# Kernel optimization log

Measured on AMD Instinct MI355X. Metric: run time of the kernel, lower is better.

The kernel has to match this reference:

```python
import jax, jax.numpy as jnp
import numpy as np

D_MODEL = 1024
N_HEADS = 16
HEAD_DIM = D_MODEL // N_HEADS


def setup_inputs() -> dict:
    key = jax.random.key(0)
    ks = jax.random.split(key, 9)
    s = 0.02
    return {
        "x": jax.random.normal(ks[0], (2, 2048, D_MODEL), jnp.float32),
        "Wk": jax.random.normal(ks[1], (D_MODEL, D_MODEL), jnp.float32) * s,
        "bk": jnp.zeros((D_MODEL,), jnp.float32),
        "Wq": jax.random.normal(ks[2], (D_MODEL, D_MODEL), jnp.float32) * s,
        "bq": jnp.zeros((D_MODEL,), jnp.float32),
        "Wv": jax.random.normal(ks[3], (D_MODEL, D_MODEL), jnp.float32) * s,
        "bv": jnp.zeros((D_MODEL,), jnp.float32),
        "Wp": jax.random.normal(ks[4], (D_MODEL, D_MODEL), jnp.float32) * s,
        "bp": jnp.zeros((D_MODEL,), jnp.float32),
    }


def reference(x, Wk, bk, Wq, bq, Wv, bv, Wp, bp):
    B, T, C = x.shape
    H, Dh = N_HEADS, HEAD_DIM
    # linear projections; torch Linear: y = x @ W.T + b
    def split_heads(y):
        return y.reshape(B, T, H, Dh).transpose(0, 2, 1, 3)  # [B,H,T,Dh]
    k = split_heads(x @ Wk.T + bk)
    q = split_heads(x @ Wq.T + bq)
    v = split_heads(x @ Wv.T + bv)
    scale = 1.0 / jnp.sqrt(jnp.asarray(Dh, x.dtype))
    att = jnp.einsum("bhqd,bhkd->bhqk", q, k) * scale  # [B,H,T,T]
    causal = jnp.tril(jnp.ones((T, T), bool))
    att = jnp.where(causal[None, None], att, -jnp.inf)
    att = jax.nn.softmax(att, axis=-1)
    y = jnp.einsum("bhqk,bhkd->bhqd", att, v)  # [B,H,T,Dh]
    y = y.transpose(0, 2, 1, 3).reshape(B, T, C)
    return y @ Wp.T + bp
```

## Files before the change

### kernel.cpp

```cpp
#include <hip/hip_runtime.h>
#include <stdint.h>

typedef unsigned short u16;
typedef __bf16 bf16x8_t __attribute__((ext_vector_type(8)));
typedef float f32x4 __attribute__((ext_vector_type(4)));

#define T_LEN 2048
#define NHEADS 16
#define DHEAD 64
#define DMODEL 1024
#define QSCALE 0.1803368801111f

__device__ __forceinline__ u16 f2bf(float f) {
  union { float f; uint32_t u; } v; v.f = f;
  uint32_t r = v.u + 0x7FFFu + ((v.u >> 16) & 1u);
  return (u16)(r >> 16);
}

__device__ __forceinline__ void gload16(const u16* g, u16* l) {
  __builtin_amdgcn_global_load_lds((const __attribute__((address_space(1))) void*)g,
                                   (__attribute__((address_space(3))) void*)l, 16, 0, 0);
}

__global__ void cvt_bf16_k(const float* __restrict__ s, u16* __restrict__ d, int n) {
  int i = (blockIdx.x * blockDim.x + threadIdx.x) * 4;
  if (i >= n) return;
  float4 f = *(const float4*)(s + i);
  u16 o[4] = { f2bf(f.x), f2bf(f.y), f2bf(f.z), f2bf(f.w) };
  *(uint2*)(d + i) = *(const uint2*)o;
}

__global__ void cvt_w_k(const float* __restrict__ wq, const float* __restrict__ wk,
                        const float* __restrict__ wv, const float* __restrict__ wp,
                        u16* __restrict__ dqkv, u16* __restrict__ dp) {
  int which = blockIdx.y;
  const float* s = which == 0 ? wq : (which == 1 ? wk : (which == 2 ? wv : wp));
  u16* d = which == 3 ? dp : dqkv + (size_t)which * 1048576;
  int i = (blockIdx.x * blockDim.x + threadIdx.x) * 4;
  float4 f = *(const float4*)(s + i);
  u16 o[4] = { f2bf(f.x), f2bf(f.y), f2bf(f.z), f2bf(f.w) };
  *(uint2*)(d + i) = *(const uint2*)o;
}

template <int TM, int TN, int MODE>
__global__ __launch_bounds__(256, 3) void gemm_k(
    const u16* __restrict__ A, const u16* __restrict__ Bw,
    const float* __restrict__ b0, const float* __restrict__ b1, const float* __restrict__ b2,
    void* __restrict__ o0, void* __restrict__ o1, void* __restrict__ o2,
    int M, int N, int K)
{
  __shared__ __align__(16) u16 As[TM][64];
  __shared__ __align__(16) u16 Bs[TN][64];
  const int m0 = blockIdx.x * TM, n0 = blockIdx.y * TN;
  const int tid = threadIdx.x, lane = tid & 63, w = tid >> 6;
  const int col = lane & 15, quad = lane >> 4;
  constexpr int WM = TM / 2, WN = TN / 2;
  const int wm = (w >> 1) * WM, wn = (w & 1) * WN;
  constexpr int NI = WM / 16, NJ = WN / 16;
  const int rsub = lane >> 3;
  const int csw = ((lane & 7) ^ rsub) * 8;
  const int rx8 = col & 7;

  f32x4 acc[NI][NJ] = {};

  for (int k0 = 0; k0 < K; k0 += 64) {
    __syncthreads();
#pragma unroll
    for (int i = 0; i < TM / 32; i++) {
      int rb = (i * 4 + w) * 8;
      gload16(&A[(size_t)(m0 + rb + rsub) * K + k0 + csw], &As[rb][0]);
    }
#pragma unroll
    for (int i = 0; i < TN / 32; i++) {
      int rb = (i * 4 + w) * 8;
      gload16(&Bw[(size_t)(n0 + rb + rsub) * K + k0 + csw], &Bs[rb][0]);
    }
    __syncthreads();
#pragma unroll
    for (int s = 0; s < 2; s++) {
      bf16x8_t af[NI], bfr[NJ];
#pragma unroll
      for (int i = 0; i < NI; i++) {
        int cp = (quad ^ rx8) ^ (s * 4);
        af[i] = *(const bf16x8_t*)&As[wm + i * 16 + col][cp * 8];
      }
#pragma unroll
      for (int j = 0; j < NJ; j++) {
        int cp = (quad ^ rx8) ^ (s * 4);
        bfr[j] = *(const bf16x8_t*)&Bs[wn + j * 16 + col][cp * 8];
      }
#pragma unroll
      for (int i = 0; i < NI; i++)
#pragma unroll
        for (int j = 0; j < NJ; j++)
          acc[i][j] = __builtin_amdgcn_mfma_f32_16x16x32_bf16(af[i], bfr[j], acc[i][j], 0, 0, 0);
    }
  }

#pragma unroll
  for (int i = 0; i < NI; i++) {
#pragma unroll
    for (int j = 0; j < NJ; j++) {
      int ncol = n0 + wn + j * 16 + col;
      if (MODE == 0) {
        float bias = b0[ncol];
#pragma unroll
        for (int r = 0; r < 4; r++) {
          int m = m0 + wm + i * 16 + quad * 4 + r;
          ((float*)o0)[(size_t)m * N + ncol] = acc[i][j][r] + bias;
        }
      } else {
        int sect = ncol >> 10, nc = ncol & 1023;
        const float* bp = sect == 0 ? b0 : (sect == 1 ? b1 : b2);
        u16* op = sect == 0 ? (u16*)o0 : (sect == 1 ? (u16*)o1 : (u16*)o2);
        float bias = bp[nc];
        float scal = sect == 0 ? QSCALE : 1.0f;
        int h = nc >> 6, d = nc & 63;
#pragma unroll
        for (int r = 0; r < 4; r++) {
          int m = m0 + wm + i * 16 + quad * 4 + r;
          int b = m >> 11, t = m & 2047;
          float v = (acc[i][j][r] + bias) * scal;
          size_t idx = sect < 2 ? ((((size_t)(b * NHEADS + h)) * T_LEN + t) * DHEAD + d)
                                : ((((size_t)(b * NHEADS + h)) * DHEAD + d) * T_LEN + t);
          op[idx] = f2bf(v);
        }
      }
    }
  }
}

__global__ __launch_bounds__(256, 3) void attn_k(
    const u16* __restrict__ Q, const u16* __restrict__ Kb,
    const u16* __restrict__ Vt, u16* __restrict__ Y)
{
  __shared__ __align__(16) u16 Ks[2][64][64];
  __shared__ __align__(16) u16 Vs[2][64][64];
  __shared__ __align__(16) u16 Ps[4][16][68];
  const int bid = blockIdx.x;
  const int bh = (bid & 7) * 4 + ((bid >> 3) & 3);
  const int qt = 31 - (bid >> 5);
  const int tid = threadIdx.x, lane = tid & 63, w = tid >> 6;
  const int col = lane & 15, quad = lane >> 4;
  const int b = bh >> 4, h = bh & 15;
  const int qw = qt * 64 + w * 16;

  const int rsub = lane >> 3;
  const int csw = ((lane & 7) ^ rsub) * 8;
  const u16* kgb = Kb + (size_t)bh * T_LEN * DHEAD;
  const u16* vgb = Vt + (size_t)bh * DHEAD * T_LEN;
  const int rx = col & 7;

  bf16x8_t qf0, qf1;
  {
    const u16* p = Q + ((size_t)bh * T_LEN + qw + col) * DHEAD + quad * 8;
    qf0 = *(const bf16x8_t*)p;
    qf1 = *(const bf16x8_t*)(p + 32);
  }

  float lsum[4] = {0.f, 0.f, 0.f, 0.f};
  f32x4 o[4] = {};
  int qrow[4];
#pragma unroll
  for (int r = 0; r < 4; r++) qrow[r] = qw + quad * 4 + r;

#pragma unroll
  for (int half = 0; half < 2; half++) {
    int rb = w * 16 + half * 8;
    gload16(kgb + (size_t)(rb + rsub) * DHEAD + csw, &Ks[0][rb][0]);
    gload16(vgb + (size_t)(rb + rsub) * T_LEN + csw, &Vs[0][rb][0]);
  }

  for (int kt = 0; kt <= qt; ++kt) {
    const int k0 = kt * 64;
    const int bufi = kt & 1;
    __syncthreads();
    if (kt < qt) {
      const int k0n = k0 + 64, bn = bufi ^ 1;
#pragma unroll
      for (int half = 0; half < 2; half++) {
        int rb = w * 16 + half * 8;
        gload16(kgb + (size_t)(k0n + rb + rsub) * DHEAD + csw, &Ks[bn][rb][0]);
        gload16(vgb + (size_t)(rb + rsub) * T_LEN + k0n + csw, &Vs[bn][rb][0]);
      }
    }

    f32x4 s[4];
#pragma unroll
    for (int nt = 0; nt < 4; nt++) {
      const u16* krow = &Ks[bufi][nt * 16 + col][0];
      bf16x8_t kf0 = *(const bf16x8_t*)(krow + ((quad ^ rx) & 7) * 8);
      bf16x8_t kf1 = *(const bf16x8_t*)(krow + (((4 + quad) ^ rx) & 7) * 8);
      f32x4 a = {};
      a = __builtin_amdgcn_mfma_f32_16x16x32_bf16(qf0, kf0, a, 0, 0, 0);
      a = __builtin_amdgcn_mfma_f32_16x16x32_bf16(qf1, kf1, a, 0, 0, 0);
      s[nt] = a;
    }

    const bool diag = (kt == qt);
#pragma unroll
    for (int r = 0; r < 4; r++) {
#pragma unroll
      for (int nt = 0; nt < 4; nt++) {
        float p = __builtin_amdgcn_exp2f(s[nt][r]);
        if (diag && (k0 + nt * 16 + col) > qrow[r]) p = 0.f;
        uint32_t pu = __float_as_uint(p) & 0xFFFF0000u;
        lsum[r] += __uint_as_float(pu);
        Ps[w][quad * 4 + r][nt * 16 + col] = (u16)(pu >> 16);
      }
    }

#pragma unroll
    for (int ks = 0; ks < 2; ks++) {
      bf16x8_t pf = *(const bf16x8_t*)&Ps[w][col][ks * 32 + quad * 8];
#pragma unroll
      for (int dt = 0; dt < 4; dt++) {
        const u16* vrow = &Vs[bufi][dt * 16 + col][0];
        bf16x8_t vv = *(const bf16x8_t*)(vrow + (((ks * 4 + quad) ^ rx) & 7) * 8);
        o[dt] = __builtin_amdgcn_mfma_f32_16x16x32_bf16(pf, vv, o[dt], 0, 0, 0);
      }
    }
  }

#pragma unroll
  for (int r = 0; r < 4; r++) {
#pragma unroll
    for (int off = 1; off < 16; off <<= 1)
      lsum[r] += __shfl_xor(lsum[r], off);
    float inv = 1.0f / lsum[r];
    int t = qw + quad * 4 + r;
#pragma unroll
    for (int dt = 0; dt < 4; dt++)
      Y[((size_t)(b * T_LEN + t)) * DMODEL + h * DHEAD + dt * 16 + col] =
          f2bf(o[dt][r] * inv);
  }
}

extern "C" void kernel_launch(void* const* d_in, const int* in_sizes, int n_in,
                              void* d_out, int out_size, void* d_ws, size_t ws_size,
                              hipStream_t stream) {
  const float* x  = (const float*)d_in[0];
  const float* Wk = (const float*)d_in[1];
  const float* bk = (const float*)d_in[2];
  const float* Wq = (const float*)d_in[3];
  const float* bq = (const float*)d_in[4];
  const float* Wv = (const float*)d_in[5];
  const float* bv = (const float*)d_in[6];
  const float* Wp = (const float*)d_in[7];
  const float* bp = (const float*)d_in[8];

  char* ws = (char*)d_ws;
  const size_t MB = 1u << 20;
  u16* xb    = (u16*)(ws);
  u16* wqkv  = (u16*)(ws + 8 * MB);
  u16* wpb   = (u16*)(ws + 14 * MB);
  u16* qb    = (u16*)(ws + 16 * MB);
  u16* kb    = (u16*)(ws + 24 * MB);
  u16* vtb   = (u16*)(ws + 32 * MB);
  u16* yatt  = (u16*)(ws + 40 * MB);

  cvt_bf16_k<<<4096, 256, 0, stream>>>(x, xb, 4194304);
  dim3 gw(1024, 4);
  cvt_w_k<<<gw, 256, 0, stream>>>(Wq, Wk, Wv, Wp, wqkv, wpb);

  dim3 gqkv(32, 24);
  gemm_k<128, 128, 3><<<gqkv, 256, 0, stream>>>(xb, wqkv, bq, bk, bv,
                                                qb, kb, vtb, 4096, 3072, 1024);

  attn_k<<<1024, 256, 0, stream>>>(qb, kb, vtb, yatt);

  dim3 gp(32, 16);
  gemm_k<128, 64, 0><<<gp, 256, 0, stream>>>(yatt, wpb, bp, nullptr, nullptr,
                                             d_out, nullptr, nullptr, 4096, 1024, 1024);
}
```

Before: 182.2 us.

## Keep attention probabilities in registers via transposed MFMA, drop LDS P staging

QK^T is now computed transposed (K as the A operand), so each lane holds the scores for one query across 16 keys. These scores are packed directly into the B operand of the PV MFMA. This removes the per-wave Ps shared-memory round trip, its write/read traffic and LDS footprint. V is now read as two 8-byte pieces per fragment to match the permuted key order, and the output is written as 4-element vector stores. Launch bounds are raised to 4 blocks per CU because shared memory is smaller, which risks register pressure or spills.

```diff
diff --git a/kernel.cpp b/kernel.cpp
--- a/kernel.cpp
+++ b/kernel.cpp
@@ -130,13 +130,12 @@
   }
 }
 
-__global__ __launch_bounds__(256, 3) void attn_k(
+__global__ __launch_bounds__(256, 4) void attn_k(
     const u16* __restrict__ Q, const u16* __restrict__ Kb,
     const u16* __restrict__ Vt, u16* __restrict__ Y)
 {
   __shared__ __align__(16) u16 Ks[2][64][64];
   __shared__ __align__(16) u16 Vs[2][64][64];
-  __shared__ __align__(16) u16 Ps[4][16][68];
   const int bid = blockIdx.x;
   const int bh = (bid & 7) * 4 + ((bid >> 3) & 3);
   const int qt = 31 - (bid >> 5);
@@ -158,11 +157,9 @@
     qf1 = *(const bf16x8_t*)(p + 32);
   }
 
-  float lsum[4] = {0.f, 0.f, 0.f, 0.f};
+  const int qr = qw + col;
+  float ls[4] = {0.f, 0.f, 0.f, 0.f};
   f32x4 o[4] = {};
-  int qrow[4];
-#pragma unroll
-  for (int r = 0; r < 4; r++) qrow[r] = qw + quad * 4 + r;
 
 #pragma unroll
   for (int half = 0; half < 2; half++) {
@@ -192,47 +189,56 @@
       bf16x8_t kf0 = *(const bf16x8_t*)(krow + ((quad ^ rx) & 7) * 8);
       bf16x8_t kf1 = *(const bf16x8_t*)(krow + (((4 + quad) ^ rx) & 7) * 8);
       f32x4 a = {};
-      a = __builtin_amdgcn_mfma_f32_16x16x32_bf16(qf0, kf0, a, 0, 0, 0);
-      a = __builtin_amdgcn_mfma_f32_16x16x32_bf16(qf1, kf1, a, 0, 0, 0);
+      a = __builtin_amdgcn_mfma_f32_16x16x32_bf16(kf0, qf0, a, 0, 0, 0);
+      a = __builtin_amdgcn_mfma_f32_16x16x32_bf16(kf1, qf1, a, 0, 0, 0);
       s[nt] = a;
     }
 
     const bool diag = (kt == qt);
+    u16 pb[4][4];
+#pragma unroll
+    for (int nt = 0; nt < 4; nt++) {
+#pragma unroll
+      for (int r = 0; r < 4; r++) {
+        float p = __builtin_amdgcn_exp2f(s[nt][r]);
+        if (diag && (k0 + nt * 16 + quad * 4 + r) > qr) p = 0.f;
+        uint32_t pu = __float_as_uint(p) & 0xFFFF0000u;
+        ls[r] += __uint_as_float(pu);
+        pb[nt][r] = (u16)(pu >> 16);
+      }
+    }
+    union PU { bf16x8_t v; u16 h[8]; } pf[2];
 #pragma unroll
     for (int r = 0; r < 4; r++) {
-#pragma unroll
-      for (int nt = 0; nt < 4; nt++) {
-        float p = __builtin_amdgcn_exp2f(s[nt][r]);
-        if (diag && (k0 + nt * 16 + col) > qrow[r]) p = 0.f;
-        uint32_t pu = __float_as_uint(p) & 0xFFFF0000u;
-        lsum[r] += __uint_as_float(pu);
-        Ps[w][quad * 4 + r][nt * 16 + col] = (u16)(pu >> 16);
-      }
+      pf[0].h[r] = pb[0][r]; pf[0].h[4 + r] = pb[1][r];
+      pf[1].h[r] = pb[2][r]; pf[1].h[4 + r] = pb[3][r];
     }
 
 #pragma unroll
     for (int ks = 0; ks < 2; ks++) {
-      bf16x8_t pf = *(const bf16x8_t*)&Ps[w][col][ks * 32 + quad * 8];
 #pragma unroll
       for (int dt = 0; dt < 4; dt++) {
         const u16* vrow = &Vs[bufi][dt * 16 + col][0];
-        bf16x8_t vv = *(const bf16x8_t*)(vrow + (((ks * 4 + quad) ^ rx) & 7) * 8);
-        o[dt] = __builtin_amdgcn_mfma_f32_16x16x32_bf16(pf, vv, o[dt], 0, 0, 0);
-      }
-    }
-  }
-
-#pragma unroll
-  for (int r = 0; r < 4; r++) {
-#pragma unroll
-    for (int off = 1; off < 16; off <<= 1)
-      lsum[r] += __shfl_xor(lsum[r], off);
-    float inv = 1.0f / lsum[r];
-    int t = qw + quad * 4 + r;
-#pragma unroll
-    for (int dt = 0; dt < 4; dt++)
-      Y[((size_t)(b * T_LEN + t)) * DMODEL + h * DHEAD + dt * 16 + col] =
-          f2bf(o[dt][r] * inv);
+        union VU { bf16x8_t v; uint2 u2[2]; } va;
+        va.u2[0] = *(const uint2*)(vrow + ((ks * 4 + (quad >> 1)) ^ rx) * 8 + (quad & 1) * 4);
+        va.u2[1] = *(const uint2*)(vrow + ((ks * 4 + 2 + (quad >> 1)) ^ rx) * 8 + (quad & 1) * 4);
+        o[dt] = __builtin_amdgcn_mfma_f32_16x16x32_bf16(va.v, pf[ks].v, o[dt], 0, 0, 0);
+      }
+    }
+  }
+
+  float lsum = (ls[0] + ls[1]) + (ls[2] + ls[3]);
+  lsum += __shfl_xor(lsum, 16);
+  lsum += __shfl_xor(lsum, 32);
+  float inv = 1.0f / lsum;
+  int t = qw + col;
+#pragma unroll
+  for (int dt = 0; dt < 4; dt++) {
+    u16 w4[4];
+#pragma unroll
+    for (int r = 0; r < 4; r++) w4[r] = f2bf(o[dt][r] * inv);
+    *(uint2*)&Y[((size_t)(b * T_LEN + t)) * DMODEL + h * DHEAD + dt * 16 + quad * 4] =
+        *(const uint2*)w4;
   }
 }
 
```

New measurement: 175.8 us. -3.5%, faster.
